# Kernel tuning notes

Hardware: AMD Instinct MI355X
Metric: run time of the kernel (lower is better)

The kernel has to match this reference:

```python
import jax, jax.numpy as jnp
import numpy as np

_Q_IN = 128          # Q7 fixed-point scale
_LUT_MIN = -1024     # covers exp(x) for x in [-8, 0]
_Q_OUT = 1 << 16     # Q16 output scale for exp LUT
_TOP_K = 2

# exp LUT: index i in [-1024, 0] -> int32(exp(i/128) * 2^16), matching _build_exp_lut
_EXP_LUT = (jnp.exp(jnp.arange(_LUT_MIN, 1, dtype=jnp.float32) / _Q_IN) * _Q_OUT).astype(jnp.int32)


def softmax_integer(logits):
    """Fixed-point INT32 softmax via Q16 exp LUT (drop-in for softmax)."""
    li = jnp.round(logits.astype(jnp.float32) * _Q_IN).astype(jnp.int32)
    shifted = jnp.clip(li - li.max(axis=-1, keepdims=True), _LUT_MIN, None)  # <= 0
    exp_vals = _EXP_LUT[shifted - _LUT_MIN]                                  # Q16 int32
    exp_sum = jnp.clip(exp_vals.sum(axis=-1, keepdims=True), 1, None)
    return exp_vals.astype(jnp.float32) / exp_sum.astype(jnp.float32)


def setup_inputs() -> dict:
    key = jax.random.key(0)
    k0, k1, k2, k3, k4 = jax.random.split(key, 5)
    B, S, H, I, E = 4, 2048, 2048, 5632, 8
    x = jax.random.normal(k0, (B, S, H), dtype=jnp.float32)
    w_gate = jax.random.normal(k1, (E, H), dtype=jnp.float32) * 0.02
    w1 = jax.random.normal(k2, (E, I, H), dtype=jnp.float32) * 0.02  # gate proj, [out,in]
    w2 = jax.random.normal(k3, (E, H, I), dtype=jnp.float32) * 0.02  # down proj
    w3 = jax.random.normal(k4, (E, I, H), dtype=jnp.float32) * 0.02  # up proj
    return {"x": x, "w_gate": w_gate, "w1": w1, "w2": w2, "w3": w3}


def reference(x, w_gate, w1, w2, w3):
    orig_shape = x.shape
    H = orig_shape[-1]
    xf = x.reshape(-1, H)                 # [T, H]
    T = xf.shape[0]
    E = w_gate.shape[0]

    router_logits = xf @ w_gate.T         # [T, E]
    routing_weights = softmax_integer(router_logits)
    top_w, top_i = jax.lax.top_k(routing_weights, _TOP_K)
    top_w = top_w / top_w.sum(axis=-1, keepdims=True)

    # dense per-(token, expert) combine weights; zero for unselected experts
    combine = jnp.zeros((T, E), xf.dtype).at[jnp.arange(T)[:, None], top_i].add(top_w)

    out = jnp.zeros_like(xf)
    for e in range(E):  # small fixed expert count
        h = jax.nn.silu(xf @ w1[e].T) * (xf @ w3[e].T)   # [T, I] SwiGLU
        out = out + combine[:, e:e + 1] * (h @ w2[e].T)  # weighted combine
    return out.reshape(orig_shape)
```

## Files before the change

kernel.cpp:

```cpp
#include <hip/hip_runtime.h>
#include <hip/hip_bf16.h>

#define T_TOK 8192
#define HD 2048
#define ID 5632
#define NE 8

typedef __bf16 bf16x8 __attribute__((ext_vector_type(8)));
typedef float f32x4 __attribute__((ext_vector_type(4)));

__global__ void k_build_lut(int* __restrict__ lut) {
    int i = blockIdx.x * blockDim.x + threadIdx.x;
    if (i <= 1024) {
        float xv = (float)(i - 1024) * (1.0f / 128.0f);
        lut[i] = (int)(expf(xv) * 65536.0f);
    }
}

__global__ __launch_bounds__(64)
void k_router(const float* __restrict__ x, const float* __restrict__ wg,
              const int* __restrict__ lut, int* __restrict__ counts,
              int* __restrict__ lists, float* __restrict__ wlist) {
    const int tok  = blockIdx.x;
    const int lane = threadIdx.x;
    const float* xr = x + (size_t)tok * HD;

    float xc[32];
    #pragma unroll
    for (int kk = 0; kk < 32; ++kk) xc[kk] = xr[lane + kk * 64];

    double dot[NE];
    #pragma unroll
    for (int e = 0; e < NE; ++e) {
        const float* wr = wg + e * HD;
        double acc = 0.0;
        #pragma unroll
        for (int kk = 0; kk < 32; ++kk)
            acc += (double)xc[kk] * (double)wr[lane + kk * 64];
        #pragma unroll
        for (int off = 32; off > 0; off >>= 1)
            acc += __shfl_down(acc, off);
        dot[e] = acc;
    }
    if (lane == 0) {
        int li[NE];
        #pragma unroll
        for (int e = 0; e < NE; ++e)
            li[e] = (int)rintf((float)dot[e] * 128.0f);
        int m = li[0];
        #pragma unroll
        for (int e = 1; e < NE; ++e) m = li[e] > m ? li[e] : m;
        int ev[NE]; int s = 0;
        #pragma unroll
        for (int e = 0; e < NE; ++e) {
            int sh = li[e] - m;
            if (sh < -1024) sh = -1024;
            ev[e] = lut[sh + 1024];
            s += ev[e];
        }
        int i0 = 0;
        #pragma unroll
        for (int e = 1; e < NE; ++e) if (ev[e] > ev[i0]) i0 = e;
        int i1 = -1;
        #pragma unroll
        for (int e = 0; e < NE; ++e) {
            if (e == i0) continue;
            if (i1 < 0 || ev[e] > ev[i1]) i1 = e;
        }
        float fs = (float)s;
        float r0 = (float)ev[i0] / fs;
        float r1 = (float)ev[i1] / fs;
        float ts = r0 + r1;
        float w0 = r0 / ts, w1 = r1 / ts;

        int p0 = atomicAdd(&counts[i0], 1);
        lists[i0 * T_TOK + p0] = (tok << 1);
        wlist[i0 * T_TOK + p0] = w0;
        int p1 = atomicAdd(&counts[i1], 1);
        lists[i1 * T_TOK + p1] = (tok << 1) | 1;
        wlist[i1 * T_TOK + p1] = w1;
    }
}

__device__ __forceinline__ bf16x8 cvt8(const float* __restrict__ s) {
    const f32x4 v0 = __builtin_nontemporal_load(reinterpret_cast<const f32x4*>(s));
    const f32x4 v1 = __builtin_nontemporal_load(reinterpret_cast<const f32x4*>(s + 4));
    bf16x8 h;
    h[0] = (__bf16)v0[0]; h[1] = (__bf16)v0[1]; h[2] = (__bf16)v0[2]; h[3] = (__bf16)v0[3];
    h[4] = (__bf16)v1[0]; h[5] = (__bf16)v1[1]; h[6] = (__bf16)v1[2]; h[7] = (__bf16)v1[3];
    return h;
}

__global__ __launch_bounds__(256)
void k_cvt_bf16(const float* __restrict__ src, __bf16* __restrict__ dst, long n8) {
    long i = (long)blockIdx.x * blockDim.x + threadIdx.x;
    const long stride = (long)gridDim.x * blockDim.x;
    for (; i < n8; i += stride)
        *reinterpret_cast<bf16x8*>(dst + i * 8) = cvt8(src + i * 8);
}

__global__ __launch_bounds__(256)
void k_cvt3_bf16(const float* __restrict__ s0, const float* __restrict__ s1, const float* __restrict__ s2,
                 __bf16* __restrict__ d0, __bf16* __restrict__ d1, __bf16* __restrict__ d2, long n8each) {
    long i = (long)blockIdx.x * blockDim.x + threadIdx.x;
    const long stride = (long)gridDim.x * blockDim.x;
    const long n2 = 2 * n8each, n3 = 3 * n8each;
    for (; i < n3; i += stride) {
        const float* src; __bf16* dst; long off;
        if (i < n8each)      { src = s0; dst = d0; off = i; }
        else if (i < n2)     { src = s1; dst = d1; off = i - n8each; }
        else                 { src = s2; dst = d2; off = i - n2; }
        *reinterpret_cast<bf16x8*>(dst + off * 8) = cvt8(src + off * 8);
    }
}

__device__ __forceinline__ void cvt_store8(void* lds_base, int woff, const float* __restrict__ src) {
    const f32x4 v0 = *reinterpret_cast<const f32x4*>(src);
    const f32x4 v1 = *reinterpret_cast<const f32x4*>(src + 4);
    bf16x8 h;
    h[0] = (__bf16)v0[0]; h[1] = (__bf16)v0[1]; h[2] = (__bf16)v0[2]; h[3] = (__bf16)v0[3];
    h[4] = (__bf16)v1[0]; h[5] = (__bf16)v1[1]; h[6] = (__bf16)v1[2]; h[7] = (__bf16)v1[3];
    *reinterpret_cast<bf16x8*>(reinterpret_cast<char*>(lds_base) + woff) = h;
}

__device__ __forceinline__ bf16x8 lds_frag(const void* lds_base, int row, int klo) {
    int off = (row * 128 + klo) ^ ((row & 7) << 4);
    return *reinterpret_cast<const bf16x8*>(reinterpret_cast<const char*>(lds_base) + off);
}

__device__ __forceinline__ void gload16(const void* g, void* l) {
    __builtin_amdgcn_global_load_lds(
        (const __attribute__((address_space(1))) unsigned int*)g,
        (__attribute__((address_space(3))) unsigned int*)l,
        16, 0, 0);
}

struct FragsA { bf16x8 a[4]; bf16x8 b1[2]; bf16x8 b3[2]; };
struct FragsB { bf16x8 a[4]; bf16x8 b[2]; };

__device__ __forceinline__ void read_fragsA(FragsA& f, const __bf16* bx, const __bf16* w1s, const __bf16* w3s,
                                            int wm, int wn, int lane, int klo) {
    #pragma unroll
    for (int m = 0; m < 4; ++m)
        f.a[m] = lds_frag(bx, wm + m * 16 + (lane & 15), klo);
    #pragma unroll
    for (int n = 0; n < 2; ++n) {
        const int r = wn + n * 16 + (lane & 15);
        f.b1[n] = lds_frag(w1s, r, klo);
        f.b3[n] = lds_frag(w3s, r, klo);
    }
}

__device__ __forceinline__ void mfmaA(f32x4 (&accg)[4][2], f32x4 (&accu)[4][2], const FragsA& f) {
    __builtin_amdgcn_s_setprio(1);
    #pragma unroll
    for (int m = 0; m < 4; ++m)
        #pragma unroll
        for (int n = 0; n < 2; ++n) {
            accg[m][n] = __builtin_amdgcn_mfma_f32_16x16x32_bf16(f.a[m], f.b1[n], accg[m][n], 0, 0, 0);
            accu[m][n] = __builtin_amdgcn_mfma_f32_16x16x32_bf16(f.a[m], f.b3[n], accu[m][n], 0, 0, 0);
        }
    __builtin_amdgcn_s_setprio(0);
}

__device__ __forceinline__ void read_fragsB(FragsB& f, const __bf16* bh, const __bf16* bw,
                                            int wm, int wn, int lane, int klo) {
    #pragma unroll
    for (int m = 0; m < 4; ++m)
        f.a[m] = lds_frag(bh, wm + m * 16 + (lane & 15), klo);
    #pragma unroll
    for (int n = 0; n < 2; ++n)
        f.b[n] = lds_frag(bw, wn + n * 16 + (lane & 15), klo);
}

__device__ __forceinline__ void mfmaB(f32x4 (&acc)[4][2], const FragsB& f) {
    __builtin_amdgcn_s_setprio(1);
    #pragma unroll
    for (int m = 0; m < 4; ++m)
        #pragma unroll
        for (int n = 0; n < 2; ++n)
            acc[m][n] = __builtin_amdgcn_mfma_f32_16x16x32_bf16(f.a[m], f.b[n], acc[m][n], 0, 0, 0);
    __builtin_amdgcn_s_setprio(0);
}


__global__ __launch_bounds__(512, 2)
void k_gateup_b16(const __bf16* __restrict__ xb, const __bf16* __restrict__ w1b,
                  const __bf16* __restrict__ w3b,
                  const int* __restrict__ counts, const int* __restrict__ lists,
                  __bf16* __restrict__ hbuf) {
    const int e   = blockIdx.z;
    const int cnt = counts[e];
    const int mt  = blockIdx.y;
    if (mt * 128 >= cnt) return;
    const int nt  = blockIdx.x;

    __shared__ __align__(16) __bf16 sX [3][8192];
    __shared__ __align__(16) __bf16 sW1[3][8192];
    __shared__ __align__(16) __bf16 sW3[3][8192];

    const int t    = threadIdx.x;
    const int lane = t & 63;
    const int wave = t >> 6;
    const int wm   = (wave >> 2) * 64;
    const int wn   = (wave & 3) * 32;

    const int lrow = lane >> 3;
    const int kel  = ((lane & 7) ^ lrow) * 8;

    const __bf16* gX[2]; const __bf16* g1[2]; const __bf16* g3[2];
    int ldo[2];
    #pragma unroll
    for (int cq = 0; cq < 2; ++cq) {
        const int c   = wave + cq * 8;
        const int row = c * 8 + lrow;
        int mi  = mt * 128 + row;
        int mic = mi < cnt - 1 ? mi : cnt - 1;
        int tok = lists[e * T_TOK + mic] >> 1;
        gX[cq] = xb + (size_t)tok * HD + kel;
        const int grow = nt * 128 + row;
        g1[cq] = w1b + ((size_t)e * ID + grow) * HD + kel;
        g3[cq] = w3b + ((size_t)e * ID + grow) * HD + kel;
        ldo[cq] = c * 1024;
    }

    f32x4 accg[4][2] = {};
    f32x4 accu[4][2] = {};

#define STAGE_A(b, kt) do { \
    _Pragma("unroll") \
    for (int cq = 0; cq < 2; ++cq) { \
        gload16(gX[cq] + (kt), (char*)sX [b] + ldo[cq]); \
        gload16(g1[cq] + (kt), (char*)sW1[b] + ldo[cq]); \
        gload16(g3[cq] + (kt), (char*)sW3[b] + ldo[cq]); \
    } } while (0)

    const int klo0 = (lane >> 4) << 4;
    const int klo1 = 64 + klo0;

    const int NT = HD / 64;
    STAGE_A(0, 0);
    STAGE_A(1, 64);
    asm volatile("s_waitcnt vmcnt(6)" ::: "memory");
    __builtin_amdgcn_s_barrier();
    __builtin_amdgcn_sched_barrier(0);

    FragsA fc, fn;
    read_fragsA(fc, sX[0], sW1[0], sW3[0], wm, wn, lane, klo0);

    for (int it = 0; it < NT - 2; ++it) {
        const int bc = it % 3, bn2 = (it + 1) % 3, bs = (it + 2) % 3;
        read_fragsA(fn, sX[bc], sW1[bc], sW3[bc], wm, wn, lane, klo1);
        STAGE_A(bs, (it + 2) * 64);
        mfmaA(accg, accu, fc);
        asm volatile("s_waitcnt vmcnt(6)" ::: "memory");
        __builtin_amdgcn_s_barrier();
        __builtin_amdgcn_sched_barrier(0);
        read_fragsA(fc, sX[bn2], sW1[bn2], sW3[bn2], wm, wn, lane, klo0);
        mfmaA(accg, accu, fn);
    }
    {
        const int bc = (NT - 2) % 3, bn2 = (NT - 1) % 3;
        read_fragsA(fn, sX[bc], sW1[bc], sW3[bc], wm, wn, lane, klo1);
        mfmaA(accg, accu, fc);
        asm volatile("s_waitcnt vmcnt(0)" ::: "memory");
        __builtin_amdgcn_s_barrier();
        __builtin_amdgcn_sched_barrier(0);
        read_fragsA(fc, sX[bn2], sW1[bn2], sW3[bn2], wm, wn, lane, klo0);
        mfmaA(accg, accu, fn);
    }
    {
        const int bc = (NT - 1) % 3;
        read_fragsA(fn, sX[bc], sW1[bc], sW3[bc], wm, wn, lane, klo1);
        mfmaA(accg, accu, fc);
        mfmaA(accg, accu, fn);
    }
#undef STAGE_A

    const int col_l = lane & 15;
    const int row_l = (lane >> 4) * 4;
    #pragma unroll
    for (int m = 0; m < 4; ++m) {
        #pragma unroll
        for (int j = 0; j < 4; ++j) {
            int tl = wm + m * 16 + row_l + j;
            int mi = mt * 128 + tl;
            if (mi < cnt) {
                int slot = lists[e * T_TOK + mi];
                __bf16* hrow = hbuf + (size_t)slot * ID + nt * 128 + wn;
                #pragma unroll
                for (int n = 0; n < 2; ++n) {
                    float g = accg[m][n][j];
                    float u = accu[m][n][j];
                    float hv = (g / (1.0f + expf(-g))) * u;
                    __builtin_nontemporal_store((__bf16)hv, &hrow[n * 16 + col_l]);
                }
            }
        }
    }
}

__global__ __launch_bounds__(512, 2)
void k_down_b16(const __bf16* __restrict__ hbuf, const __bf16* __restrict__ w2b,
                const int* __restrict__ counts, const int* __restrict__ lists,
                const float* __restrict__ wlist, float* __restrict__ out) {
    const int e   = blockIdx.z;
    const int cnt = counts[e];
    const int mt  = blockIdx.y;
    if (mt * 128 >= cnt) return;
    const int nt  = blockIdx.x;

    __shared__ __align__(16) __bf16 sH[3][8192];
    __shared__ __align__(16) __bf16 sW[3][8192];

    const int t    = threadIdx.x;
    const int lane = t & 63;
    const int wave = t >> 6;
    const int wm   = (wave >> 2) * 64;
    const int wn   = (wave & 3) * 32;

    const int lrow = lane >> 3;
    const int kel  = ((lane & 7) ^ lrow) * 8;

    const __bf16* gH[2]; const __bf16* gW[2];
    int ldo[2];
    #pragma unroll
    for (int cq = 0; cq < 2; ++cq) {
        const int c   = wave + cq * 8;
        const int row = c * 8 + lrow;
        int mi  = mt * 128 + row;
        int mic = mi < cnt - 1 ? mi : cnt - 1;
        int slot = lists[e * T_TOK + mic];
        gH[cq] = hbuf + (size_t)slot * ID + kel;
        const int grow = nt * 128 + row;
        gW[cq] = w2b + ((size_t)e * HD + grow) * ID + kel;
        ldo[cq] = c * 1024;
    }

    f32x4 acc[4][2] = {};

#define STAGE_B(b, kt) do { \
    _Pragma("unroll") \
    for (int cq = 0; cq < 2; ++cq) { \
        gload16(gH[cq] + (kt), (char*)sH[b] + ldo[cq]); \
        gload16(gW[cq] + (kt), (char*)sW[b] + ldo[cq]); \
    } } while (0)

    const int klo0 = (lane >> 4) << 4;
    const int klo1 = 64 + klo0;

    const int NT = ID / 64;
    STAGE_B(0, 0);
    STAGE_B(1, 64);
    asm volatile("s_waitcnt vmcnt(4)" ::: "memory");
    __builtin_amdgcn_s_barrier();
    __builtin_amdgcn_sched_barrier(0);

    FragsB fc, fn;
    read_fragsB(fc, sH[0], sW[0], wm, wn, lane, klo0);

    for (int it = 0; it < NT - 2; ++it) {
        const int bc = it % 3, bn2 = (it + 1) % 3, bs = (it + 2) % 3;
        read_fragsB(fn, sH[bc], sW[bc], wm, wn, lane, klo1);
        STAGE_B(bs, (it + 2) * 64);
        mfmaB(acc, fc);
        asm volatile("s_waitcnt vmcnt(4)" ::: "memory");
        __builtin_amdgcn_s_barrier();
        __builtin_amdgcn_sched_barrier(0);
        read_fragsB(fc, sH[bn2], sW[bn2], wm, wn, lane, klo0);
        mfmaB(acc, fn);
    }
    {
        const int bc = (NT - 2) % 3, bn2 = (NT - 1) % 3;
        read_fragsB(fn, sH[bc], sW[bc], wm, wn, lane, klo1);
        mfmaB(acc, fc);
        asm volatile("s_waitcnt vmcnt(0)" ::: "memory");
        __builtin_amdgcn_s_barrier();
        __builtin_amdgcn_sched_barrier(0);
        read_fragsB(fc, sH[bn2], sW[bn2], wm, wn, lane, klo0);
        mfmaB(acc, fn);
    }
    {
        const int bc = (NT - 1) % 3;
        read_fragsB(fn, sH[bc], sW[bc], wm, wn, lane, klo1);
        mfmaB(acc, fc);
        mfmaB(acc, fn);
    }
#undef STAGE_B

    const int col_l = lane & 15;
    const int row_l = (lane >> 4) * 4;
    #pragma unroll
    for (int m = 0; m < 4; ++m) {
        #pragma unroll
        for (int j = 0; j < 4; ++j) {
            int tl = wm + m * 16 + row_l + j;
            int mi = mt * 128 + tl;
            if (mi < cnt) {
                int slot = lists[e * T_TOK + mi];
                int tok  = slot >> 1;
                float w  = wlist[e * T_TOK + mi];
                float* orow = out + (size_t)tok * HD + nt * 128 + wn;
                #pragma unroll
                for (int n = 0; n < 2; ++n)
                    atomicAdd(&orow[n * 16 + col_l], w * acc[m][n][j]);
            }
        }
    }
}


__global__ __launch_bounds__(256)
void k_gateup_f32(const float* __restrict__ x, const float* __restrict__ w1,
                  const float* __restrict__ w3,
                  const int* __restrict__ counts, const int* __restrict__ lists,
                  __bf16* __restrict__ hbuf) {
    const int e   = blockIdx.z;
    const int cnt = counts[e];
    const int mt  = blockIdx.y;
    if (mt * 128 >= cnt) return;
    const int nt  = blockIdx.x;

    __shared__ __align__(16) __bf16 sX [128 * 64];
    __shared__ __align__(16) __bf16 sW1[128 * 64];
    __shared__ __align__(16) __bf16 sW3[128 * 64];

    const int t    = threadIdx.x;
    const int lane = t & 63;
    const int wave = t >> 6;
    const int wm   = (wave >> 1) * 64;
    const int wn   = (wave & 1) * 64;
    const int cc = t & 7;
    const int r0 = t >> 3;

    const float* srcX[4]; const float* src1[4]; const float* src3[4];
    int woff[4];
    #pragma unroll
    for (int q = 0; q < 4; ++q) {
        int row = r0 + 32 * q;
        int mi  = mt * 128 + row;
        int mic = mi < cnt - 1 ? mi : cnt - 1;
        int slot = lists[e * T_TOK + mic];
        int tok  = slot >> 1;
        srcX[q] = x + (size_t)tok * HD + cc * 8;
        int grow = nt * 128 + row;
        src1[q] = w1 + ((size_t)e * ID + grow) * HD + cc * 8;
        src3[q] = w3 + ((size_t)e * ID + grow) * HD + cc * 8;
        woff[q] = (row * 128 + cc * 16) ^ ((row & 7) << 4);
    }

    f32x4 accg[4][4] = {};
    f32x4 accu[4][4] = {};

    for (int kt = 0; kt < HD; kt += 64) {
        __syncthreads();
        #pragma unroll
        for (int q = 0; q < 4; ++q) {
            cvt_store8(sX,  woff[q], srcX[q] + kt);
            cvt_store8(sW1, woff[q], src1[q] + kt);
            cvt_store8(sW3, woff[q], src3[q] + kt);
        }
        __syncthreads();
        #pragma unroll
        for (int kk = 0; kk < 2; ++kk) {
            const int klo = kk * 64 + ((lane >> 4) << 4);
            bf16x8 af[4], b1f[4], b3f[4];
            #pragma unroll
            for (int m = 0; m < 4; ++m)
                af[m] = lds_frag(sX, wm + m * 16 + (lane & 15), klo);
            #pragma unroll
            for (int n = 0; n < 4; ++n) {
                int row = wn + n * 16 + (lane & 15);
                b1f[n] = lds_frag(sW1, row, klo);
                b3f[n] = lds_frag(sW3, row, klo);
            }
            #pragma unroll
            for (int m = 0; m < 4; ++m)
                #pragma unroll
                for (int n = 0; n < 4; ++n) {
                    accg[m][n] = __builtin_amdgcn_mfma_f32_16x16x32_bf16(af[m], b1f[n], accg[m][n], 0, 0, 0);
                    accu[m][n] = __builtin_amdgcn_mfma_f32_16x16x32_bf16(af[m], b3f[n], accu[m][n], 0, 0, 0);
                }
        }
    }

    const int col_l = lane & 15;
    const int row_l = (lane >> 4) * 4;
    #pragma unroll
    for (int m = 0; m < 4; ++m) {
        #pragma unroll
        for (int j = 0; j < 4; ++j) {
            int tl = wm + m * 16 + row_l + j;
            int mi = mt * 128 + tl;
            if (mi < cnt) {
                int slot = lists[e * T_TOK + mi];
                __bf16* hrow = hbuf + (size_t)slot * ID + nt * 128 + wn;
                #pragma unroll
                for (int n = 0; n < 4; ++n) {
                    float g = accg[m][n][j];
                    float u = accu[m][n][j];
                    float hv = (g / (1.0f + expf(-g))) * u;
                    hrow[n * 16 + col_l] = (__bf16)hv;
                }
            }
        }
    }
}

__global__ __launch_bounds__(256)
void k_down_f32(const __bf16* __restrict__ hbuf, const float* __restrict__ w2,
                const int* __restrict__ counts, const int* __restrict__ lists,
                const float* __restrict__ wlist, float* __restrict__ out) {
    const int e   = blockIdx.z;
    const int cnt = counts[e];
    const int mt  = blockIdx.y;
    if (mt * 128 >= cnt) return;
    const int nt  = blockIdx.x;

    __shared__ __align__(16) __bf16 sH[128 * 64];
    __shared__ __align__(16) __bf16 sW[128 * 64];

    const int t    = threadIdx.x;
    const int lane = t & 63;
    const int wave = t >> 6;
    const int wm   = (wave >> 1) * 64;
    const int wn   = (wave & 1) * 64;
    const int cc = t & 7;
    const int r0 = t >> 3;

    const __bf16* srcH[4]; const float* srcW[4];
    int woff[4];
    #pragma unroll
    for (int q = 0; q < 4; ++q) {
        int row = r0 + 32 * q;
        int mi  = mt * 128 + row;
        int mic = mi < cnt - 1 ? mi : cnt - 1;
        int slot = lists[e * T_TOK + mic];
        srcH[q] = hbuf + (size_t)slot * ID + cc * 8;
        int grow = nt * 128 + row;
        srcW[q] = w2 + ((size_t)e * HD + grow) * ID + cc * 8;
        woff[q] = (row * 128 + cc * 16) ^ ((row & 7) << 4);
    }

    f32x4 acc[4][4] = {};

    for (int kt = 0; kt < ID; kt += 64) {
        __syncthreads();
        #pragma unroll
        for (int q = 0; q < 4; ++q) {
            bf16x8 v = *reinterpret_cast<const bf16x8*>(srcH[q] + kt);
            *reinterpret_cast<bf16x8*>(reinterpret_cast<char*>(sH) + woff[q]) = v;
            cvt_store8(sW, woff[q], srcW[q] + kt);
        }
        __syncthreads();
        #pragma unroll
        for (int kk = 0; kk < 2; ++kk) {
            const int klo = kk * 64 + ((lane >> 4) << 4);
            bf16x8 af[4], bf[4];
            #pragma unroll
            for (int m = 0; m < 4; ++m)
                af[m] = lds_frag(sH, wm + m * 16 + (lane & 15), klo);
            #pragma unroll
            for (int n = 0; n < 4; ++n)
                bf[n] = lds_frag(sW, wn + n * 16 + (lane & 15), klo);
            #pragma unroll
            for (int m = 0; m < 4; ++m)
                #pragma unroll
                for (int n = 0; n < 4; ++n)
                    acc[m][n] = __builtin_amdgcn_mfma_f32_16x16x32_bf16(af[m], bf[n], acc[m][n], 0, 0, 0);
        }
    }

    const int col_l = lane & 15;
    const int row_l = (lane >> 4) * 4;
    #pragma unroll
    for (int m = 0; m < 4; ++m) {
        #pragma unroll
        for (int j = 0; j < 4; ++j) {
            int tl = wm + m * 16 + row_l + j;
            int mi = mt * 128 + tl;
            if (mi < cnt) {
                int slot = lists[e * T_TOK + mi];
                int tok  = slot >> 1;
                float w  = wlist[e * T_TOK + mi];
                float* orow = out + (size_t)tok * HD + nt * 128 + wn;
                #pragma unroll
                for (int n = 0; n < 4; ++n)
                    atomicAdd(&orow[n * 16 + col_l], w * acc[m][n][j]);
            }
        }
    }
}

extern "C" void kernel_launch(void* const* d_in, const int* in_sizes, int n_in,
                              void* d_out, int out_size, void* d_ws, size_t ws_size,
                              hipStream_t stream) {
    const float* x  = (const float*)d_in[0];
    const float* wg = (const float*)d_in[1];
    const float* w1 = (const float*)d_in[2];
    const float* w2 = (const float*)d_in[3];
    const float* w3 = (const float*)d_in[4];
    float* out = (float*)d_out;

    const size_t HBUF_B = (size_t)2 * T_TOK * ID * 2;
    const size_t XB_B   = (size_t)T_TOK * HD * 2;
    const size_t WB_B   = (size_t)NE * ID * HD * 2;
    const size_t SMALL  = 4608 + 512 + (size_t)NE * T_TOK * 4 * 2 + 4096;

    char* ws = (char*)d_ws;
    __bf16* hbuf = (__bf16*)ws;

    const size_t XB_OFF  = HBUF_B;
    const size_t W1_OFF  = XB_OFF + XB_B;
    const size_t W3_OFF  = W1_OFF + WB_B;
    const size_t W2_OFF  = W3_OFF + WB_B;
    const size_t TAIL    = W2_OFF + WB_B;
    const size_t NEED_FULL = TAIL + SMALL;
    const size_t NEED_MIN  = HBUF_B + SMALL;

    if (ws_size >= NEED_FULL) {
        __bf16* xb  = (__bf16*)(ws + XB_OFF);
        __bf16* w1b = (__bf16*)(ws + W1_OFF);
        __bf16* w3b = (__bf16*)(ws + W3_OFF);
        __bf16* w2b = (__bf16*)(ws + W2_OFF);
        int*   lut    = (int*)(ws + TAIL);
        int*   counts = (int*)(ws + TAIL + 4608);
        int*   lists  = (int*)(ws + TAIL + 4608 + 512);
        float* wlist  = (float*)(ws + TAIL + 4608 + 512 + (size_t)NE * T_TOK * 4);

        (void)hipMemsetAsync(out, 0, (size_t)out_size * sizeof(float), stream);
        (void)hipMemsetAsync(counts, 0, 64, stream);
        k_build_lut<<<dim3(5), dim3(256), 0, stream>>>(lut);
        k_router<<<dim3(T_TOK), dim3(64), 0, stream>>>(x, wg, lut, counts, lists, wlist);
        k_cvt_bf16<<<dim3(1024), dim3(256), 0, stream>>>(x, xb, (long)T_TOK * HD / 8);
        k_cvt3_bf16<<<dim3(4096), dim3(256), 0, stream>>>(w1, w3, w2, w1b, w3b, w2b, (long)NE * ID * HD / 8);
        k_gateup_b16<<<dim3(ID / 128, T_TOK / 128, NE), dim3(512), 0, stream>>>(xb, w1b, w3b, counts, lists, hbuf);
        k_down_b16<<<dim3(HD / 128, T_TOK / 128, NE), dim3(512), 0, stream>>>(hbuf, w2b, counts, lists, wlist, out);
    } else if (ws_size >= NEED_MIN) {
        int*   lut    = (int*)(ws + HBUF_B);
        int*   counts = (int*)(ws + HBUF_B + 4608);
        int*   lists  = (int*)(ws + HBUF_B + 4608 + 512);
        float* wlist  = (float*)(ws + HBUF_B + 4608 + 512 + (size_t)NE * T_TOK * 4);

        (void)hipMemsetAsync(out, 0, (size_t)out_size * sizeof(float), stream);
        (void)hipMemsetAsync(counts, 0, 64, stream);
        k_build_lut<<<dim3(5), dim3(256), 0, stream>>>(lut);
        k_router<<<dim3(T_TOK), dim3(64), 0, stream>>>(x, wg, lut, counts, lists, wlist);
        k_gateup_f32<<<dim3(ID / 128, T_TOK / 128, NE), dim3(256), 0, stream>>>(x, w1, w3, counts, lists, hbuf);
        k_down_f32<<<dim3(HD / 128, T_TOK / 128, NE), dim3(256), 0, stream>>>(hbuf, w2, counts, lists, wlist, out);
    } else {
        (void)hipMemsetAsync(d_out, 0x7F, (size_t)out_size * sizeof(float), stream);
    }
}
```

Baseline: 2.108 ms.

## Enlarge down-proj tile to 256 tokens with 64x64 warp tiles

The down-projection kernel now processes 256 routed tokens per block instead of 128. Each wave computes a 64x64 output tile, so every loaded W2 tile is reused across twice as many tokens and the number of MFMAs per LDS fragment read goes up. The cost is more accumulator registers, larger LDS buffers and fewer blocks, which may hurt occupancy at 2 blocks per CU and leave more padding waste on partially filled expert tiles. The wait instructions now also include lgkmcnt(0), and the h stores in gate-up change from nontemporal to normal stores.

```diff
diff --git a/kernel.cpp b/kernel.cpp
--- a/kernel.cpp
+++ b/kernel.cpp
@@ -136,7 +136,7 @@
 }
 
 struct FragsA { bf16x8 a[4]; bf16x8 b1[2]; bf16x8 b3[2]; };
-struct FragsB { bf16x8 a[4]; bf16x8 b[2]; };
+struct FragsB { bf16x8 a[4]; bf16x8 b[4]; };
 
 __device__ __forceinline__ void read_fragsA(FragsA& f, const __bf16* bx, const __bf16* w1s, const __bf16* w3s,
                                             int wm, int wn, int lane, int klo) {
@@ -169,16 +169,16 @@
     for (int m = 0; m < 4; ++m)
         f.a[m] = lds_frag(bh, wm + m * 16 + (lane & 15), klo);
     #pragma unroll
-    for (int n = 0; n < 2; ++n)
+    for (int n = 0; n < 4; ++n)
         f.b[n] = lds_frag(bw, wn + n * 16 + (lane & 15), klo);
 }
 
-__device__ __forceinline__ void mfmaB(f32x4 (&acc)[4][2], const FragsB& f) {
+__device__ __forceinline__ void mfmaB(f32x4 (&acc)[4][4], const FragsB& f) {
     __builtin_amdgcn_s_setprio(1);
     #pragma unroll
     for (int m = 0; m < 4; ++m)
         #pragma unroll
-        for (int n = 0; n < 2; ++n)
+        for (int n = 0; n < 4; ++n)
             acc[m][n] = __builtin_amdgcn_mfma_f32_16x16x32_bf16(f.a[m], f.b[n], acc[m][n], 0, 0, 0);
     __builtin_amdgcn_s_setprio(0);
 }
@@ -241,7 +241,7 @@
     const int NT = HD / 64;
     STAGE_A(0, 0);
     STAGE_A(1, 64);
-    asm volatile("s_waitcnt vmcnt(6)" ::: "memory");
+    asm volatile("s_waitcnt vmcnt(6) lgkmcnt(0)" ::: "memory");
     __builtin_amdgcn_s_barrier();
     __builtin_amdgcn_sched_barrier(0);
 
@@ -253,7 +253,7 @@
         read_fragsA(fn, sX[bc], sW1[bc], sW3[bc], wm, wn, lane, klo1);
         STAGE_A(bs, (it + 2) * 64);
         mfmaA(accg, accu, fc);
-        asm volatile("s_waitcnt vmcnt(6)" ::: "memory");
+        asm volatile("s_waitcnt vmcnt(6) lgkmcnt(0)" ::: "memory");
         __builtin_amdgcn_s_barrier();
         __builtin_amdgcn_sched_barrier(0);
         read_fragsA(fc, sX[bn2], sW1[bn2], sW3[bn2], wm, wn, lane, klo0);
@@ -263,7 +263,7 @@
         const int bc = (NT - 2) % 3, bn2 = (NT - 1) % 3;
         read_fragsA(fn, sX[bc], sW1[bc], sW3[bc], wm, wn, lane, klo1);
         mfmaA(accg, accu, fc);
-        asm volatile("s_waitcnt vmcnt(0)" ::: "memory");
+        asm volatile("s_waitcnt vmcnt(0) lgkmcnt(0)" ::: "memory");
         __builtin_amdgcn_s_barrier();
         __builtin_amdgcn_sched_barrier(0);
         read_fragsA(fc, sX[bn2], sW1[bn2], sW3[bn2], wm, wn, lane, klo0);
@@ -293,7 +293,7 @@
                     float g = accg[m][n][j];
                     float u = accu[m][n][j];
                     float hv = (g / (1.0f + expf(-g))) * u;
-                    __builtin_nontemporal_store((__bf16)hv, &hrow[n * 16 + col_l]);
+                    hrow[n * 16 + col_l] = (__bf16)hv;
                 }
             }
         }
@@ -307,44 +307,50 @@
     const int e   = blockIdx.z;
     const int cnt = counts[e];
     const int mt  = blockIdx.y;
-    if (mt * 128 >= cnt) return;
+    if (mt * 256 >= cnt) return;
     const int nt  = blockIdx.x;
 
-    __shared__ __align__(16) __bf16 sH[3][8192];
-    __shared__ __align__(16) __bf16 sW[3][8192];
+    __shared__ __align__(16) __bf16 sH[3][256 * 64];
+    __shared__ __align__(16) __bf16 sW[3][128 * 64];
 
     const int t    = threadIdx.x;
     const int lane = t & 63;
     const int wave = t >> 6;
-    const int wm   = (wave >> 2) * 64;
-    const int wn   = (wave & 3) * 32;
+    const int wm   = (wave >> 1) * 64;
+    const int wn   = (wave & 1) * 64;
 
     const int lrow = lane >> 3;
     const int kel  = ((lane & 7) ^ lrow) * 8;
 
-    const __bf16* gH[2]; const __bf16* gW[2];
-    int ldo[2];
-    #pragma unroll
-    for (int cq = 0; cq < 2; ++cq) {
-        const int c   = wave + cq * 8;
+    const __bf16* gH[4]; int loH[4];
+    #pragma unroll
+    for (int q = 0; q < 4; ++q) {
+        const int c   = wave + q * 8;
         const int row = c * 8 + lrow;
-        int mi  = mt * 128 + row;
+        int mi  = mt * 256 + row;
         int mic = mi < cnt - 1 ? mi : cnt - 1;
         int slot = lists[e * T_TOK + mic];
-        gH[cq] = hbuf + (size_t)slot * ID + kel;
+        gH[q]  = hbuf + (size_t)slot * ID + kel;
+        loH[q] = c * 1024;
+    }
+    const __bf16* gW[2]; int loW[2];
+    #pragma unroll
+    for (int q = 0; q < 2; ++q) {
+        const int c   = wave + q * 8;
+        const int row = c * 8 + lrow;
         const int grow = nt * 128 + row;
-        gW[cq] = w2b + ((size_t)e * HD + grow) * ID + kel;
-        ldo[cq] = c * 1024;
-    }
-
-    f32x4 acc[4][2] = {};
+        gW[q]  = w2b + ((size_t)e * HD + grow) * ID + kel;
+        loW[q] = c * 1024;
+    }
+
+    f32x4 acc[4][4] = {};
 
 #define STAGE_B(b, kt) do { \
     _Pragma("unroll") \
-    for (int cq = 0; cq < 2; ++cq) { \
-        gload16(gH[cq] + (kt), (char*)sH[b] + ldo[cq]); \
-        gload16(gW[cq] + (kt), (char*)sW[b] + ldo[cq]); \
-    } } while (0)
+    for (int q = 0; q < 4; ++q) gload16(gH[q] + (kt), (char*)sH[b] + loH[q]); \
+    _Pragma("unroll") \
+    for (int q = 0; q < 2; ++q) gload16(gW[q] + (kt), (char*)sW[b] + loW[q]); \
+    } while (0)
 
     const int klo0 = (lane >> 4) << 4;
     const int klo1 = 64 + klo0;
@@ -352,7 +358,7 @@
     const int NT = ID / 64;
     STAGE_B(0, 0);
     STAGE_B(1, 64);
-    asm volatile("s_waitcnt vmcnt(4)" ::: "memory");
+    asm volatile("s_waitcnt vmcnt(6) lgkmcnt(0)" ::: "memory");
     __builtin_amdgcn_s_barrier();
     __builtin_amdgcn_sched_barrier(0);
 
@@ -364,7 +370,7 @@
         read_fragsB(fn, sH[bc], sW[bc], wm, wn, lane, klo1);
         STAGE_B(bs, (it + 2) * 64);
         mfmaB(acc, fc);
-        asm volatile("s_waitcnt vmcnt(4)" ::: "memory");
+        asm volatile("s_waitcnt vmcnt(6) lgkmcnt(0)" ::: "memory");
         __builtin_amdgcn_s_barrier();
         __builtin_amdgcn_sched_barrier(0);
         read_fragsB(fc, sH[bn2], sW[bn2], wm, wn, lane, klo0);
@@ -374,7 +380,7 @@
         const int bc = (NT - 2) % 3, bn2 = (NT - 1) % 3;
         read_fragsB(fn, sH[bc], sW[bc], wm, wn, lane, klo1);
         mfmaB(acc, fc);
-        asm volatile("s_waitcnt vmcnt(0)" ::: "memory");
+        asm volatile("s_waitcnt vmcnt(0) lgkmcnt(0)" ::: "memory");
         __builtin_amdgcn_s_barrier();
         __builtin_amdgcn_sched_barrier(0);
         read_fragsB(fc, sH[bn2], sW[bn2], wm, wn, lane, klo0);
@@ -395,14 +401,14 @@
         #pragma unroll
         for (int j = 0; j < 4; ++j) {
             int tl = wm + m * 16 + row_l + j;
-            int mi = mt * 128 + tl;
+            int mi = mt * 256 + tl;
             if (mi < cnt) {
                 int slot = lists[e * T_TOK + mi];
                 int tok  = slot >> 1;
                 float w  = wlist[e * T_TOK + mi];
                 float* orow = out + (size_t)tok * HD + nt * 128 + wn;
                 #pragma unroll
-                for (int n = 0; n < 2; ++n)
+                for (int n = 0; n < 4; ++n)
                     atomicAdd(&orow[n * 16 + col_l], w * acc[m][n][j]);
             }
         }
@@ -635,7 +641,7 @@
         k_cvt_bf16<<<dim3(1024), dim3(256), 0, stream>>>(x, xb, (long)T_TOK * HD / 8);
         k_cvt3_bf16<<<dim3(4096), dim3(256), 0, stream>>>(w1, w3, w2, w1b, w3b, w2b, (long)NE * ID * HD / 8);
         k_gateup_b16<<<dim3(ID / 128, T_TOK / 128, NE), dim3(512), 0, stream>>>(xb, w1b, w3b, counts, lists, hbuf);
-        k_down_b16<<<dim3(HD / 128, T_TOK / 128, NE), dim3(512), 0, stream>>>(hbuf, w2b, counts, lists, wlist, out);
+        k_down_b16<<<dim3(HD / 128, T_TOK / 256, NE), dim3(512), 0, stream>>>(hbuf, w2b, counts, lists, wlist, out);
     } else if (ws_size >= NEED_MIN) {
         int*   lut    = (int*)(ws + HBUF_B);
         int*   counts = (int*)(ws + HBUF_B + 4608);
```

Result: faster. 1.999 ms, median of 2 (-5.2%).
